# Kernel tuning notes

Measured on AMD Instinct MI355X. Metric: run time of the kernel, lower is better.

Reference implementation:

```python
import jax, jax.numpy as jnp
import numpy as np

B, NQ, NK = 4, 2048, 2048
CQ, CK = 1024, 768
H = 16
D = CQ // H  # 64
EPS = 1e-5


def layernorm(x, gamma, beta):
    mu = jnp.mean(x, axis=-1, keepdims=True)
    var = jnp.var(x, axis=-1, keepdims=True)
    return (x - mu) * jax.lax.rsqrt(var + EPS) * gamma + beta


def setup_inputs() -> dict:
    key = jax.random.key(0)
    ks = jax.random.split(key, 12)
    s_q = 1.0 / np.sqrt(CQ)
    s_c = 1.0 / np.sqrt(CK)
    return {
        "query_tokens": jax.random.normal(ks[0], (B, NQ, CQ), jnp.float32),
        "context_tokens": jax.random.normal(ks[1], (B, NK, CK), jnp.float32),
        "Wq": jax.random.uniform(ks[2], (CQ, CQ), jnp.float32, -s_q, s_q),
        "bq": jnp.zeros((CQ,), jnp.float32),
        "Wk": jax.random.uniform(ks[3], (CK, CQ), jnp.float32, -s_c, s_c),
        "bk": jnp.zeros((CQ,), jnp.float32),
        "Wv": jax.random.uniform(ks[4], (CK, CQ), jnp.float32, -s_c, s_c),
        "bv": jnp.zeros((CQ,), jnp.float32),
        "Wo": jax.random.uniform(ks[5], (CQ, CQ), jnp.float32, -s_q, s_q),
        "bo": jnp.zeros((CQ,), jnp.float32),
        "gamma_q": jnp.ones((CQ,), jnp.float32),
        "beta_q": jnp.zeros((CQ,), jnp.float32),
        "gamma_ctx": jnp.ones((CK,), jnp.float32),
        "beta_ctx": jnp.zeros((CK,), jnp.float32),
    }


def reference(query_tokens, context_tokens, Wq, bq, Wk, bk, Wv, bv, Wo, bo,
              gamma_q, beta_q, gamma_ctx, beta_ctx):
    scale = 1.0 / np.sqrt(D)
    xq = layernorm(query_tokens, gamma_q, beta_q)      # [B,NQ,CQ]
    xc = layernorm(context_tokens, gamma_ctx, beta_ctx)  # [B,NK,CK]
    q = (xq @ Wq + bq).reshape(B, NQ, H, D)
    k = (xc @ Wk + bk).reshape(B, NK, H, D)
    v = (xc @ Wv + bv).reshape(B, NK, H, D)
    scores = jnp.einsum('bqhd,bkhd->bhqk', q, k) * scale  # [B,H,NQ,NK]
    attn = jax.nn.softmax(scores, axis=-1)
    attended = jnp.einsum('bhqk,bkhd->bqhd', attn, v).reshape(B, NQ, CQ)
    return attended @ Wo + bo
```

## Files before the change

kernel.cpp:

```cpp
#include <hip/hip_runtime.h>
#include <hip/hip_bf16.h>
#include <stdint.h>

#define B_    4
#define NQ_   2048
#define NK_   2048
#define CQ_   1024
#define CK_   768
#define H_    16
#define D_    64
#define SCALE 0.125f
#define C2    0.1803368801111204f

typedef __attribute__((ext_vector_type(8))) short bf16x8;
typedef __attribute__((ext_vector_type(4))) float f32x4;
typedef __attribute__((ext_vector_type(4))) unsigned int u32x4;

#define MFMA16(a, b, c) __builtin_amdgcn_mfma_f32_16x16x32_bf16((a), (b), (c), 0, 0, 0)

#define GLL16(gp, lp)                                                                 \
    __builtin_amdgcn_global_load_lds(                                                 \
        (__attribute__((address_space(1))) uint32_t*)(uintptr_t)(gp),                 \
        (__attribute__((address_space(3))) uint32_t*)(uintptr_t)(lp), 16, 0, 0)

__device__ inline unsigned short f2bf(float f) {
    union { float f; uint32_t u; } v; v.f = f;
    uint32_t u = v.u;
    return (unsigned short)((u + 0x7fffu + ((u >> 16) & 1u)) >> 16);
}

__device__ inline uint32_t packbf2(float a, float b) {
    union { __hip_bfloat162 h; uint32_t u; } v;
    v.h = __float22bfloat162_rn(float2{a, b});
    return v.u;
}

__global__ __launch_bounds__(256) void ln_tr(const float* __restrict__ xqt,
                                             const float* __restrict__ xct,
                                             const float* __restrict__ gq,
                                             const float* __restrict__ btq,
                                             const float* __restrict__ gc,
                                             const float* __restrict__ btc,
                                             unsigned short* __restrict__ oq,
                                             unsigned short* __restrict__ oc,
                                             const float* __restrict__ Wq,
                                             const float* __restrict__ Wk,
                                             const float* __restrict__ Wv,
                                             const float* __restrict__ Wo,
                                             unsigned short* __restrict__ Wqt,
                                             unsigned short* __restrict__ Wkvt,
                                             unsigned short* __restrict__ Wot) {
    __shared__ float red[8];
    __shared__ float stat[2];
    __shared__ float tt[32][33];
    int blk = blockIdx.x;
    int tid = threadIdx.x;

    if (blk < 16384) {
        const float *x, *gamma, *beta;
        unsigned short* out;
        int W;
        float invW;
        if (blk < 8192) {
            x = xqt + (size_t)blk * 1024; gamma = gq; beta = btq;
            out = oq + (size_t)blk * 1024; W = 1024; invW = 1.f / 1024.f;
        } else {
            int r = blk - 8192;
            x = xct + (size_t)r * 768; gamma = gc; beta = btc;
            out = oc + (size_t)r * 768; W = 768; invW = 1.f / 768.f;
        }
        int col = tid * 4;
        float v0 = 0.f, v1 = 0.f, v2 = 0.f, v3 = 0.f;
        float s = 0.f, s2 = 0.f;
        bool active = (col < W);
        if (active) {
            float4 vv = *(const float4*)(x + col);
            v0 = vv.x; v1 = vv.y; v2 = vv.z; v3 = vv.w;
            s = v0 + v1 + v2 + v3;
            s2 = v0 * v0 + v1 * v1 + v2 * v2 + v3 * v3;
        }
        for (int off = 32; off >= 1; off >>= 1) {
            s += __shfl_xor(s, off);
            s2 += __shfl_xor(s2, off);
        }
        int wid = tid >> 6, lane = tid & 63;
        if (lane == 0) { red[wid] = s; red[4 + wid] = s2; }
        __syncthreads();
        if (tid == 0) {
            float ts = red[0] + red[1] + red[2] + red[3];
            float ts2 = red[4] + red[5] + red[6] + red[7];
            float mu = ts * invW;
            float var = ts2 * invW - mu * mu;
            stat[0] = mu;
            stat[1] = rsqrtf(var + 1e-5f);
        }
        __syncthreads();
        float mu = stat[0], rstd = stat[1];
        if (active) {
            float4 gm = *(const float4*)(gamma + col);
            float4 bt = *(const float4*)(beta + col);
            ushort4 o;
            o.x = f2bf((v0 - mu) * rstd * gm.x + bt.x);
            o.y = f2bf((v1 - mu) * rstd * gm.y + bt.y);
            o.z = f2bf((v2 - mu) * rstd * gm.z + bt.z);
            o.w = f2bf((v3 - mu) * rstd * gm.w + bt.w);
            *(ushort4*)(out + col) = o;
        }
    } else {
        int b2 = blk - 16384;
        const float* src;
        unsigned short* dst;
        int K;
        if (b2 < 1024)      { src = Wq; dst = Wqt; K = 1024; }
        else if (b2 < 1792) { b2 -= 1024; src = Wk; dst = Wkvt; K = 768; }
        else if (b2 < 2560) { b2 -= 1792; src = Wv; dst = Wkvt + (size_t)1024 * 768; K = 768; }
        else                 { b2 -= 2560; src = Wo; dst = Wot; K = 1024; }
        int n0 = (b2 & 31) * 32, k0 = (b2 >> 5) * 32;
        int tx = tid & 31, ty = tid >> 5;
        for (int i = 0; i < 4; i++)
            tt[ty + 8 * i][tx] = src[(size_t)(k0 + ty + 8 * i) * 1024 + n0 + tx];
        __syncthreads();
        for (int i = 0; i < 4; i++)
            dst[(size_t)(n0 + ty + 8 * i) * K + k0 + tx] = f2bf(tt[tx][ty + 8 * i]);
    }
}

__global__ __launch_bounds__(256) void gemm_qkv(const unsigned short* __restrict__ xq,
                                                const unsigned short* __restrict__ Wqt,
                                                const float* __restrict__ bq,
                                                const unsigned short* __restrict__ xc,
                                                const unsigned short* __restrict__ Wkvt,
                                                const float* __restrict__ bk,
                                                const float* __restrict__ bv,
                                                unsigned short* __restrict__ Qb,
                                                unsigned short* __restrict__ Kb,
                                                unsigned short* __restrict__ Vtb) {
    __shared__ __align__(16) unsigned short As[4][128 * 32];
    __shared__ __align__(16) unsigned short Bs[4][128 * 32];
    int tid = threadIdx.x;
    int lane = tid & 63, wid = tid >> 6;
    int q = lane & 15, g = lane >> 4;

    int lin = blockIdx.x;
    int xcd = lin & 7;
    int idx = lin >> 3;
    const unsigned short *X, *Wt;
    int Kd, NB, sub, qrole;
    if (idx < 64) { X = xq; Wt = Wqt;  Kd = 1024; NB = 8;  sub = xcd * 64 + idx;          qrole = 1; }
    else          { X = xc; Wt = Wkvt; Kd = 768;  NB = 16; sub = xcd * 128 + (idx - 64);  qrole = 0; }
    int m0 = (sub / NB) * 128;
    int n0 = (sub % NB) * 128;
    int wm = wid >> 1, wn = wid & 1;

    f32x4 acc[4][4];
    for (int i = 0; i < 4; i++)
        for (int j = 0; j < 4; j++) acc[i][j] = (f32x4){0.f, 0.f, 0.f, 0.f};

    int sx2 = (((lane & 3) ^ ((lane >> 2) & 3)) << 4);
    int srow0 = wid * 32 + (lane >> 2);
    const char* Xb = (const char*)X;
    const char* Wb = (const char*)Wt;
    char* AsB = (char*)As;
    char* BsB = (char*)Bs;

    auto STAGE = [&](int buf, int t) {
#pragma unroll
        for (int c = 0; c < 2; c++) {
            int row = srow0 + c * 16;
            GLL16(Xb + ((size_t)(m0 + row) * Kd + t * 32) * 2 + sx2,
                  AsB + buf * 8192 + wid * 2048 + c * 1024);
            GLL16(Wb + ((size_t)(n0 + row) * Kd + t * 32) * 2 + sx2,
                  BsB + buf * 8192 + wid * 2048 + c * 1024);
        }
    };

    int ck = (g ^ (q & 3)) << 4;
    auto COMPUTE = [&](int buf) {
        bf16x8 a[4], b[4];
#pragma unroll
        for (int mf = 0; mf < 4; mf++)
            a[mf] = *(const bf16x8*)(AsB + buf * 8192 + (wm * 64 + mf * 16 + q) * 64 + ck);
#pragma unroll
        for (int nf = 0; nf < 4; nf++)
            b[nf] = *(const bf16x8*)(BsB + buf * 8192 + (wn * 64 + nf * 16 + q) * 64 + ck);
#pragma unroll
        for (int mf = 0; mf < 4; mf++)
#pragma unroll
            for (int nf = 0; nf < 4; nf++) acc[mf][nf] = MFMA16(a[mf], b[nf], acc[mf][nf]);
    };

    int nT = Kd >> 5;
    STAGE(0, 0);
    STAGE(1, 1);
    STAGE(2, 2);
    STAGE(3, 3);
    __syncthreads();

    for (int i = 0; i < nT / 2; i++) {
        int t = 2 * i;
        COMPUTE(t & 3);
        COMPUTE((t + 1) & 3);
        __syncthreads();
        if (t + 4 < nT) {
            STAGE(t & 3, t + 4);
            STAGE((t + 1) & 3, t + 5);
        }
    }

    int crow0 = m0 + wm * 64;
    int ccol0 = n0 + wn * 64;
    for (int nf = 0; nf < 4; nf++) {
        int col = ccol0 + nf * 16 + q;
        float bv_ = qrole ? bq[col] : ((col < 1024) ? bk[col] : bv[col - 1024]);
        if (!qrole && col >= 1024) {
            int c = col - 1024;
            int h = c >> 6, d = c & 63;
            for (int mf = 0; mf < 4; mf++) {
                int rowb = crow0 + mf * 16 + g * 4;
                int b = rowb >> 11;
                int nqb = rowb & 2047;
                int u = nqb & 63;
                int pbase = (nqb & ~63) | ((u & 32) + ((u & 12) << 1) + ((u & 16) >> 2));
                ushort4 o;
                o.x = f2bf(acc[mf][nf][0] + bv_);
                o.y = f2bf(acc[mf][nf][1] + bv_);
                o.z = f2bf(acc[mf][nf][2] + bv_);
                o.w = f2bf(acc[mf][nf][3] + bv_);
                *(ushort4*)&Vtb[(((size_t)(b * H_ + h)) * 64 + d) * NK_ + pbase] = o;
            }
        } else {
            for (int mf = 0; mf < 4; mf++) {
                int rowb = crow0 + mf * 16 + g * 4;
                for (int r = 0; r < 4; r++) {
                    int row = rowb + r;
                    float val = acc[mf][nf][r] + bv_;
                    int b = row >> 11, nq = row & 2047;
                    int h = col >> 6, d = col & 63;
                    if (qrole) {
                        Qb[(((size_t)(b * H_ + h)) * NQ_ + nq) * 64 + d] = f2bf(val * C2);
                    } else {
                        Kb[(((size_t)(b * H_ + h)) * NQ_ + nq) * 64 + d] = f2bf(val);
                    }
                }
            }
        }
    }
}

__global__ __launch_bounds__(256) void gemm_out(const unsigned short* __restrict__ X,
                                                const unsigned short* __restrict__ Wt,
                                                const float* __restrict__ bias0,
                                                float* __restrict__ out0) {
    __shared__ __align__(16) unsigned short As[4][128 * 32];
    __shared__ __align__(16) unsigned short Bs[4][128 * 32];
    int tid = threadIdx.x;
    int lane = tid & 63, wid = tid >> 6;
    int q = lane & 15, g = lane >> 4;
    const int Kd = 1024;

    int lin = blockIdx.y * 8 + blockIdx.x;
    int virt = (lin & 7) * 64 + (lin >> 3);
    int m0 = (virt / 8) * 128;
    int n0 = (virt % 8) * 128;
    int wm = wid >> 1, wn = wid & 1;

    f32x4 acc[4][4];
    for (int i = 0; i < 4; i++)
        for (int j = 0; j < 4; j++) acc[i][j] = (f32x4){0.f, 0.f, 0.f, 0.f};

    int sx2 = (((lane & 3) ^ ((lane >> 2) & 3)) << 4);
    int srow0 = wid * 32 + (lane >> 2);
    const char* Xb = (const char*)X;
    const char* Wb = (const char*)Wt;
    char* AsB = (char*)As;
    char* BsB = (char*)Bs;

    auto STAGE = [&](int buf, int t) {
#pragma unroll
        for (int c = 0; c < 2; c++) {
            int row = srow0 + c * 16;
            GLL16(Xb + ((size_t)(m0 + row) * Kd + t * 32) * 2 + sx2,
                  AsB + buf * 8192 + wid * 2048 + c * 1024);
            GLL16(Wb + ((size_t)(n0 + row) * Kd + t * 32) * 2 + sx2,
                  BsB + buf * 8192 + wid * 2048 + c * 1024);
        }
    };

    int ck = (g ^ (q & 3)) << 4;
    auto COMPUTE = [&](int buf) {
        bf16x8 a[4], b[4];
#pragma unroll
        for (int mf = 0; mf < 4; mf++)
            a[mf] = *(const bf16x8*)(AsB + buf * 8192 + (wm * 64 + mf * 16 + q) * 64 + ck);
#pragma unroll
        for (int nf = 0; nf < 4; nf++)
            b[nf] = *(const bf16x8*)(BsB + buf * 8192 + (wn * 64 + nf * 16 + q) * 64 + ck);
#pragma unroll
        for (int mf = 0; mf < 4; mf++)
#pragma unroll
            for (int nf = 0; nf < 4; nf++) acc[mf][nf] = MFMA16(a[mf], b[nf], acc[mf][nf]);
    };

    const int nT = 32;
    STAGE(0, 0);
    STAGE(1, 1);
    STAGE(2, 2);
    STAGE(3, 3);
    __syncthreads();

    for (int i = 0; i < nT / 2; i++) {
        int t = 2 * i;
        COMPUTE(t & 3);
        COMPUTE((t + 1) & 3);
        __syncthreads();
        if (t + 4 < nT) {
            STAGE(t & 3, t + 4);
            STAGE((t + 1) & 3, t + 5);
        }
    }

    int crow0 = m0 + wm * 64;
    int ccol0 = n0 + wn * 64;
    for (int nf = 0; nf < 4; nf++) {
        int col = ccol0 + nf * 16 + q;
        float bv_ = bias0[col];
        for (int mf = 0; mf < 4; mf++) {
            int rowb = crow0 + mf * 16 + g * 4;
            for (int r = 0; r < 4; r++) {
                int row = rowb + r;
                out0[(size_t)row * 1024 + col] = acc[mf][nf][r] + bv_;
            }
        }
    }
}

__global__ __launch_bounds__(512, 4) void flash_attn(const unsigned short* __restrict__ Q,
                                                     const unsigned short* __restrict__ K,
                                                     const unsigned short* __restrict__ Vt,
                                                     unsigned short* __restrict__ attended) {
    __shared__ __align__(16) char smem[4][16384];
    int tid = threadIdx.x, lane = tid & 63, wid = tid >> 6;
    int g = lane >> 4;
    int q = lane & 15;

    const f32x4 zero4 = {0.f, 0.f, 0.f, 0.f};

    int lin = blockIdx.y * 8 + blockIdx.x;
    int virt = (lin & 7) * 64 + (lin >> 3);
    int bh = virt >> 3;
    int q0 = (virt & 7) * 256;
    const char* Qb = (const char*)(Q + (size_t)bh * NQ_ * 64);
    const char* Kb = (const char*)(K + (size_t)bh * NK_ * 64);
    const char* Vb = (const char*)(Vt + (size_t)bh * 64 * NK_);

    int qrow = q0 + wid * 32 + q;
    bf16x8 qf0[2], qf1[2];
    qf0[0] = *(const bf16x8*)(Qb + (size_t)qrow * 128 + g * 16);
    qf0[1] = *(const bf16x8*)(Qb + (size_t)qrow * 128 + g * 16 + 64);
    qf1[0] = *(const bf16x8*)(Qb + (size_t)(qrow + 16) * 128 + g * 16);
    qf1[1] = *(const bf16x8*)(Qb + (size_t)(qrow + 16) * 128 + g * 16 + 64);

    bf16x8 onesf;
#pragma unroll
    for (int i = 0; i < 8; i++) onesf[i] = (short)0x3f80;

    f32x4 acc0[4], acc1[4];
    for (int i = 0; i < 4; i++) {
        acc0[i] = zero4;
        acc1[i] = zero4;
    }
    f32x4 accl0 = zero4, accl1 = zero4;

    int sxor = ((lane & 7) * 16) ^ (((lane >> 3) & 7) << 4);
    const char* kptr = Kb + (size_t)(wid * 8 + (lane >> 3)) * 128 + sxor;
    const char* vptr = Vb + (size_t)(wid * 8 + (lane >> 3)) * 4096 + sxor;
    int cb0 = g * 16;
    int swz = (lane & 7) << 4;

    auto TILE = [&](const char* Ksb, const char* Vsb) {
        f32x4 s0[4], s1[4];
        __builtin_amdgcn_s_setprio(1);
#pragma unroll
        for (int nf = 0; nf < 4; nf++) {
            bf16x8 kf0 = *(const bf16x8*)(Ksb + (nf * 16 + q) * 128 + (cb0 ^ swz));
            bf16x8 kf1 = *(const bf16x8*)(Ksb + (nf * 16 + q) * 128 + ((cb0 + 64) ^ swz));
            s0[nf] = MFMA16(kf0, qf0[0], zero4);
            s0[nf] = MFMA16(kf1, qf0[1], s0[nf]);
            s1[nf] = MFMA16(kf0, qf1[0], zero4);
            s1[nf] = MFMA16(kf1, qf1[1], s1[nf]);
        }
        __builtin_amdgcn_s_setprio(0);

        __builtin_amdgcn_s_setprio(1);
#pragma unroll
        for (int kk = 0; kk < 2; kk++) {
            float p0v[8], p1v[8];
#pragma unroll
            for (int h = 0; h < 2; h++)
#pragma unroll
                for (int r = 0; r < 4; r++) {
                    p0v[4 * h + r] = __builtin_amdgcn_exp2f(s0[2 * kk + h][r]);
                    p1v[4 * h + r] = __builtin_amdgcn_exp2f(s1[2 * kk + h][r]);
                }
            union { u32x4 u; bf16x8 b; } ap0, ap1;
            ap0.u[0] = packbf2(p0v[0], p0v[1]);
            ap0.u[1] = packbf2(p0v[2], p0v[3]);
            ap0.u[2] = packbf2(p0v[4], p0v[5]);
            ap0.u[3] = packbf2(p0v[6], p0v[7]);
            ap1.u[0] = packbf2(p1v[0], p1v[1]);
            ap1.u[1] = packbf2(p1v[2], p1v[3]);
            ap1.u[2] = packbf2(p1v[4], p1v[5]);
            ap1.u[3] = packbf2(p1v[6], p1v[7]);

            accl0 = MFMA16(ap0.b, onesf, accl0);
            accl1 = MFMA16(ap1.b, onesf, accl1);
#pragma unroll
            for (int df = 0; df < 4; df++) {
                bf16x8 bv = *(const bf16x8*)(Vsb + (df * 16 + q) * 128 + ((cb0 + kk * 64) ^ swz));
                acc0[df] = MFMA16(ap0.b, bv, acc0[df]);
                acc1[df] = MFMA16(ap1.b, bv, acc1[df]);
            }
        }
        __builtin_amdgcn_s_setprio(0);
    };

#pragma unroll
    for (int j = 0; j < 4; j++) {
        GLL16(kptr, smem[j] + wid * 1024);
        GLL16(vptr, smem[j] + 8192 + wid * 1024);
        kptr += 8192;
        vptr += 128;
    }
    __syncthreads();

    for (int i = 0; i < 16; ++i) {
        int t = 2 * i;
        const char* B0 = smem[t & 3];
        const char* B1 = smem[(t + 1) & 3];
        TILE(B0, B0 + 8192);
        TILE(B1, B1 + 8192);
        __syncthreads();
        if (t + 4 < 32) {
            GLL16(kptr, smem[t & 3] + wid * 1024);
            GLL16(vptr, smem[t & 3] + 8192 + wid * 1024);
            kptr += 8192;
            vptr += 128;
            GLL16(kptr, smem[(t + 1) & 3] + wid * 1024);
            GLL16(vptr, smem[(t + 1) & 3] + 8192 + wid * 1024);
            kptr += 8192;
            vptr += 128;
        }
    }

    int b = bh >> 4, h = bh & 15;
#pragma unroll
    for (int df = 0; df < 4; df++)
#pragma unroll
        for (int r = 0; r < 4; r++) {
            int row = q0 + wid * 32 + 4 * g + r;
            int col = h * 64 + df * 16 + q;
            attended[(size_t)(b * NQ_ + row) * CQ_ + col] = f2bf(acc0[df][r] / accl0[r]);
            attended[(size_t)(b * NQ_ + row + 16) * CQ_ + col] = f2bf(acc1[df][r] / accl1[r]);
        }
}

extern "C" void kernel_launch(void* const* d_in, const int* in_sizes, int n_in,
                              void* d_out, int out_size, void* d_ws, size_t ws_size,
                              hipStream_t stream) {
    const float* qt  = (const float*)d_in[0];
    const float* ct  = (const float*)d_in[1];
    const float* Wq  = (const float*)d_in[2];
    const float* bq  = (const float*)d_in[3];
    const float* Wk  = (const float*)d_in[4];
    const float* bk  = (const float*)d_in[5];
    const float* Wv  = (const float*)d_in[6];
    const float* bv  = (const float*)d_in[7];
    const float* Wo  = (const float*)d_in[8];
    const float* bo  = (const float*)d_in[9];
    const float* gq  = (const float*)d_in[10];
    const float* btq = (const float*)d_in[11];
    const float* gc  = (const float*)d_in[12];
    const float* btc = (const float*)d_in[13];

    char* ws = (char*)d_ws;
    unsigned short* xq   = (unsigned short*)(ws + 0);
    unsigned short* xc   = (unsigned short*)(ws + 16777216);
    unsigned short* Wqt  = (unsigned short*)(ws + 29360128);
    unsigned short* Wkvt = (unsigned short*)(ws + 31457280);
    unsigned short* Wot  = (unsigned short*)(ws + 34603008);
    unsigned short* Qb   = (unsigned short*)(ws + 36700160);
    unsigned short* Kb   = (unsigned short*)(ws + 53477376);
    unsigned short* Vtb  = (unsigned short*)(ws + 70254592);

    ln_tr<<<19968, 256, 0, stream>>>(qt, ct, gq, btq, gc, btc, xq, xc,
                                     Wq, Wk, Wv, Wo, Wqt, Wkvt, Wot);

    gemm_qkv<<<1536, 256, 0, stream>>>(xq, Wqt, bq, xc, Wkvt, bk, bv, Qb, Kb, Vtb);

    flash_attn<<<dim3(8, 64), 512, 0, stream>>>(Qb, Kb, Vtb, xq);

    gemm_out<<<dim3(8, 64), 256, 0, stream>>>(xq, Wot, bo, (float*)d_out);
}
```

Baseline: 177.1 us.

## Enlarge QKV GEMM tile to 128x256 with 512 threads, single-buffered K=64 loop

```diff
diff --git a/kernel.cpp b/kernel.cpp
--- a/kernel.cpp
+++ b/kernel.cpp
@@ -125,7 +125,7 @@
     }
 }
 
-__global__ __launch_bounds__(256) void gemm_qkv(const unsigned short* __restrict__ xq,
+__global__ __launch_bounds__(512) void gemm_qkv(const unsigned short* __restrict__ xq,
                                                 const unsigned short* __restrict__ Wqt,
                                                 const float* __restrict__ bq,
                                                 const unsigned short* __restrict__ xc,
@@ -135,8 +135,8 @@
                                                 unsigned short* __restrict__ Qb,
                                                 unsigned short* __restrict__ Kb,
                                                 unsigned short* __restrict__ Vtb) {
-    __shared__ __align__(16) unsigned short As[4][128 * 32];
-    __shared__ __align__(16) unsigned short Bs[4][128 * 32];
+    __shared__ __align__(16) unsigned short As[128 * 64];
+    __shared__ __align__(16) unsigned short Bs[256 * 64];
     int tid = threadIdx.x;
     int lane = tid & 63, wid = tid >> 6;
     int q = lane & 15, g = lane >> 4;
@@ -146,65 +146,52 @@
     int idx = lin >> 3;
     const unsigned short *X, *Wt;
     int Kd, NB, sub, qrole;
-    if (idx < 64) { X = xq; Wt = Wqt;  Kd = 1024; NB = 8;  sub = xcd * 64 + idx;          qrole = 1; }
-    else          { X = xc; Wt = Wkvt; Kd = 768;  NB = 16; sub = xcd * 128 + (idx - 64);  qrole = 0; }
+    if (idx < 32) { X = xq; Wt = Wqt;  Kd = 1024; NB = 4; sub = xcd * 32 + idx;         qrole = 1; }
+    else          { X = xc; Wt = Wkvt; Kd = 768;  NB = 8; sub = xcd * 64 + (idx - 32);  qrole = 0; }
     int m0 = (sub / NB) * 128;
-    int n0 = (sub % NB) * 128;
-    int wm = wid >> 1, wn = wid & 1;
+    int n0 = (sub % NB) * 256;
+    int wm = wid >> 2, wn = wid & 3;
 
     f32x4 acc[4][4];
     for (int i = 0; i < 4; i++)
         for (int j = 0; j < 4; j++) acc[i][j] = (f32x4){0.f, 0.f, 0.f, 0.f};
 
-    int sx2 = (((lane & 3) ^ ((lane >> 2) & 3)) << 4);
-    int srow0 = wid * 32 + (lane >> 2);
+    int srow = wid * 8 + (lane >> 3);
+    int sxor = ((lane & 7) * 16) ^ (((lane >> 3) & 7) << 4);
+    int swz = (lane & 7) << 4;
     const char* Xb = (const char*)X;
     const char* Wb = (const char*)Wt;
     char* AsB = (char*)As;
     char* BsB = (char*)Bs;
 
-    auto STAGE = [&](int buf, int t) {
-#pragma unroll
-        for (int c = 0; c < 2; c++) {
-            int row = srow0 + c * 16;
-            GLL16(Xb + ((size_t)(m0 + row) * Kd + t * 32) * 2 + sx2,
-                  AsB + buf * 8192 + wid * 2048 + c * 1024);
-            GLL16(Wb + ((size_t)(n0 + row) * Kd + t * 32) * 2 + sx2,
-                  BsB + buf * 8192 + wid * 2048 + c * 1024);
-        }
-    };
-
-    int ck = (g ^ (q & 3)) << 4;
-    auto COMPUTE = [&](int buf) {
-        bf16x8 a[4], b[4];
-#pragma unroll
-        for (int mf = 0; mf < 4; mf++)
-            a[mf] = *(const bf16x8*)(AsB + buf * 8192 + (wm * 64 + mf * 16 + q) * 64 + ck);
-#pragma unroll
-        for (int nf = 0; nf < 4; nf++)
-            b[nf] = *(const bf16x8*)(BsB + buf * 8192 + (wn * 64 + nf * 16 + q) * 64 + ck);
-#pragma unroll
-        for (int mf = 0; mf < 4; mf++)
-#pragma unroll
-            for (int nf = 0; nf < 4; nf++) acc[mf][nf] = MFMA16(a[mf], b[nf], acc[mf][nf]);
-    };
-
-    int nT = Kd >> 5;
-    STAGE(0, 0);
-    STAGE(1, 1);
-    STAGE(2, 2);
-    STAGE(3, 3);
-    __syncthreads();
-
-    for (int i = 0; i < nT / 2; i++) {
-        int t = 2 * i;
-        COMPUTE(t & 3);
-        COMPUTE((t + 1) & 3);
-        __syncthreads();
-        if (t + 4 < nT) {
-            STAGE(t & 3, t + 4);
-            STAGE((t + 1) & 3, t + 5);
-        }
+    for (int k0 = 0; k0 < Kd; k0 += 64) {
+#pragma unroll
+        for (int i = 0; i < 2; i++) {
+            int row = i * 64 + srow;
+            GLL16(Xb + ((size_t)(m0 + row) * Kd + k0) * 2 + sxor, AsB + i * 8192 + wid * 1024);
+        }
+#pragma unroll
+        for (int i = 0; i < 4; i++) {
+            int row = i * 64 + srow;
+            GLL16(Wb + ((size_t)(n0 + row) * Kd + k0) * 2 + sxor, BsB + i * 8192 + wid * 1024);
+        }
+        __syncthreads();
+#pragma unroll
+        for (int kk = 0; kk < 2; kk++) {
+            int cb = ((g * 16 + kk * 64) ^ swz);
+            bf16x8 a[4], b[4];
+#pragma unroll
+            for (int mf = 0; mf < 4; mf++)
+                a[mf] = *(const bf16x8*)(AsB + (wm * 64 + mf * 16 + q) * 128 + cb);
+#pragma unroll
+            for (int nf = 0; nf < 4; nf++)
+                b[nf] = *(const bf16x8*)(BsB + (wn * 64 + nf * 16 + q) * 128 + cb);
+#pragma unroll
+            for (int mf = 0; mf < 4; mf++)
+#pragma unroll
+                for (int nf = 0; nf < 4; nf++) acc[mf][nf] = MFMA16(a[mf], b[nf], acc[mf][nf]);
+        }
+        __syncthreads();
     }
 
     int crow0 = m0 + wm * 64;
@@ -495,7 +482,7 @@
     ln_tr<<<19968, 256, 0, stream>>>(qt, ct, gq, btq, gc, btc, xq, xc,
                                      Wq, Wk, Wv, Wo, Wqt, Wkvt, Wot);
 
-    gemm_qkv<<<1536, 256, 0, stream>>>(xq, Wqt, bq, xc, Wkvt, bk, bv, Qb, Kb, Vtb);
+    gemm_qkv<<<768, 512, 0, stream>>>(xq, Wqt, bq, xc, Wkvt, bk, bv, Qb, Kb, Vtb);
 
     flash_attn<<<dim3(8, 64), 512, 0, stream>>>(Qb, Kb, Vtb, xq);
 
```

Result: faster. 169.1 us, median of 2 (-4.6%).
